# Optimization experiments

Hardware: AMD Instinct MI355X
Metric: run time of the kernel (lower is better)

Reference implementation:

```python
import jax, jax.numpy as jnp
import numpy as np
import math


def setup_inputs() -> dict:
    key = jax.random.key(0)
    ks = jax.random.split(key, 5)
    B, L, H = 16384, 336, 168
    T = L + H
    T_air = jax.random.normal(ks[0], (B, T), dtype=jnp.float32) * 8.0 + 10.0
    T_obs = T_air + jax.random.normal(ks[1], (B, T), dtype=jnp.float32) * 2.0
    wind = jax.random.uniform(ks[2], (B, T), dtype=jnp.float32) * 10.0
    par = jax.random.uniform(ks[3], (B, T), dtype=jnp.float32) * 500.0
    dt = jax.random.uniform(ks[4], (B, T), dtype=jnp.float32) * 3600.0 + 1800.0
    k_init = 1e-4
    k_raw = jnp.float32(k_init + math.log(-math.expm1(-k_init)))  # softplus inverse
    return {
        "T_obs": T_obs, "T_air": T_air, "wind": wind, "par": par, "dt": dt,
        "L_hist": L,
        "k_raw": k_raw,
        "log_q": jnp.float32(-8.0), "log_r": jnp.float32(-4.0),
        "log_p0": jnp.float32(-2.0), "log_q_scale": jnp.float32(0.0),
        "theta_par_lin": jnp.float32(1e-5), "theta_par_quad": jnp.float32(1e-8),
        "theta_wind_cool": jnp.float32(-1e-5), "theta_sensible": jnp.float32(-1e-6),
        "theta_forced_conv": jnp.float32(-1e-7),
    }


def reference(T_obs, T_air, wind, par, dt, L_hist, k_raw, log_q, log_r, log_p0,
              log_q_scale, theta_par_lin, theta_par_quad, theta_wind_cool,
              theta_sensible, theta_forced_conv):
    B, T_total = T_obs.shape
    L = int(L_hist)
    H = T_total - L

    k = jax.nn.softplus(k_raw)
    q = jnp.exp(log_q)
    q_scale = jnp.exp(log_q_scale)
    R = jnp.exp(log_r)
    P0 = jnp.exp(log_p0)

    def predict(T, P, Ta, w, p, dtt):
        dT = T - Ta
        cl = (theta_par_lin * p + theta_par_quad * p * p + theta_wind_cool * w
              + theta_sensible * dT + theta_forced_conv * w * dT)
        T_pred = jnp.clip(T - k * dT * dtt + cl * dtt, -50.0, 100.0)
        F = jnp.clip(1.0 - k * dtt + (theta_sensible + theta_forced_conv * w) * dtt, -2.0, 2.0)
        P_pred = jnp.clip(F * F * P + q_scale * q * dtt, 1e-10, 1e6)
        return T_pred, P_pred

    def filt_step(carry, xs):
        T, P = carry
        Ta, w, p, dtt, y = xs
        Tp, Pp = predict(T, P, Ta, w, p, dtt)
        S = Pp + R
        K = Pp / S
        T_upd = Tp + K * (y - Tp)
        P_upd = (1.0 - K) ** 2 * Pp + K * K * R
        return (T_upd, P_upd), None

    s0 = T_obs[:, 0]
    P0b = jnp.broadcast_to(P0, (B,)).astype(T_obs.dtype)

    # filtering over t = 1 .. L-1 (forcing from t-1, dt/obs at t)
    filt_xs = (T_air[:, :L - 1].T, wind[:, :L - 1].T, par[:, :L - 1].T,
               jnp.clip(dt[:, 1:L], 1.0, None).T, T_obs[:, 1:L].T)
    (s, P), _ = jax.lax.scan(filt_step, (s0, P0b), filt_xs)

    def fcst_step(carry, xs):
        T, P = carry
        Ta, w, p, dtt = xs
        Tp, Pp = predict(T, P, Ta, w, p, dtt)
        return (Tp, Pp), (Tp, Pp)

    # open-loop forecast over t = L .. L+H-1 (forcing from idx-1)
    fcst_xs = (T_air[:, L - 1:L + H - 1].T, wind[:, L - 1:L + H - 1].T,
               par[:, L - 1:L + H - 1].T, jnp.clip(dt[:, L:], 1.0, None).T)
    _, (T_preds, T_vars) = jax.lax.scan(fcst_step, (s, P), fcst_xs)

    return T_preds.T, T_vars.T  # each [B, H]
```

## Files before the change

kernel.cpp:

```cpp
#include <hip/hip_runtime.h>
#include <hip/hip_fp16.h>

namespace {
constexpr int kB = 16384;
constexpr int kL = 336;
constexpr int kH = 168;
constexpr int kT = 504;
constexpr int kW = 16;
constexpr int kNW = 32;
constexpr int kFW = 21;
constexpr int kNB = 4;
constexpr int kTP = 8;
constexpr int kS2 = 65;
constexpr int kTile2 = kTP * kS2;
constexpr int kOS = 17;
constexpr int kOT = 64 * kOS;
}

__device__ inline int fwaitc(int* f, int target, int cached) {
    if (cached >= target) { asm volatile("" ::: "memory"); return cached; }
    int v, guard = 0;
    while ((v = __hip_atomic_load(f, __ATOMIC_RELAXED, __HIP_MEMORY_SCOPE_WORKGROUP)) < target) {
        __builtin_amdgcn_s_sleep(1);
        if (++guard > (1 << 22)) { v = target; break; }
    }
    asm volatile("" ::: "memory");
    return v;
}
__device__ inline void fpost(int* f, int lane) {
    asm volatile("s_waitcnt lgkmcnt(0)" ::: "memory");
    if (lane == 0)
        __hip_atomic_fetch_add(f, 1, __ATOMIC_RELAXED, __HIP_MEMORY_SCOPE_WORKGROUP);
}

__global__ __launch_bounds__(256, 1)
void kf_fused(const float* __restrict__ g_obs,
              const float* __restrict__ g_air,
              const float* __restrict__ g_wind,
              const float* __restrict__ g_par,
              const float* __restrict__ g_dt,
              const float* __restrict__ s_k_raw,
              const float* __restrict__ s_log_q,
              const float* __restrict__ s_log_r,
              const float* __restrict__ s_log_p0,
              const float* __restrict__ s_log_qs,
              const float* __restrict__ s_th_pl,
              const float* __restrict__ s_th_pq,
              const float* __restrict__ s_th_wc,
              const float* __restrict__ s_th_s,
              const float* __restrict__ s_th_fc,
              float* __restrict__ out)
{
    __shared__ __half2 s_in[5][kNB][kTile2];
    __shared__ float   s_oT[2][kOT];
    __shared__ float   s_oV[2][kOT];
    __shared__ int     s_flag[8];

    const int tid = threadIdx.x, wid = tid >> 6, lane = tid & 63;
    const int b0 = blockIdx.x * 64;

    if (tid < 8) s_flag[tid] = 0;
    __syncthreads();

    int* pcAW = &s_flag[0];
    int* pcPD = &s_flag[1];
    int* pcY  = &s_flag[2];
    int* cc   = &s_flag[3];
    int* sc   = &s_flag[4];

    const int iq = lane & 3;
    const int ir = lane >> 2;

    auto issue = [&](const float* __restrict__ g, int w, float4* r) {
        int t = w * kW + iq * 4;
        if (t > kT - 4) t = kT - 4;
#pragma unroll
        for (int i = 0; i < 4; ++i)
            r[i] = *(const float4*)(g + (size_t)(b0 + 16 * i + ir) * kT + t);
    };
    auto stash = [&](const float4* r, __half2* dst) {
#pragma unroll
        for (int i = 0; i < 4; ++i) {
            const int row = 16 * i + ir;
            dst[(iq * 2    ) * kS2 + row] = __floats2half2_rn(r[i].x, r[i].y);
            dst[(iq * 2 + 1) * kS2 + row] = __floats2half2_rn(r[i].z, r[i].w);
        }
    };

    if (wid == 1 || wid == 2) {
        const float* g0 = (wid == 1) ? g_air  : g_par;
        const float* g1 = (wid == 1) ? g_wind : g_dt;
        __half2* t0b = (wid == 1) ? &s_in[0][0][0] : &s_in[2][0][0];
        __half2* t1b = (wid == 1) ? &s_in[1][0][0] : &s_in[3][0][0];
        int* pc = (wid == 1) ? pcAW : pcPD;

        float4 a0[4], c0[4], a1[4], c1[4];
        issue(g0, 0, a0); issue(g1, 0, c0);
        issue(g0, 1, a1); issue(g1, 1, c1);
        __builtin_amdgcn_sched_barrier(0);
        int vcc = 0;
        for (int w = 0; w < kNW; ++w) {
            if (w >= kNB) vcc = fwaitc(cc, w - (kNB - 1), vcc);
            const int bi = w & 3;
            if (w & 1) {
                stash(a1, t0b + bi * kTile2); stash(c1, t1b + bi * kTile2);
                fpost(pc, lane);
                if (w + 2 < kNW) { issue(g0, w + 2, a1); issue(g1, w + 2, c1); }
            } else {
                stash(a0, t0b + bi * kTile2); stash(c0, t1b + bi * kTile2);
                fpost(pc, lane);
                if (w + 2 < kNW) { issue(g0, w + 2, a0); issue(g1, w + 2, c0); }
            }
            __builtin_amdgcn_sched_barrier(0);
        }
    } else if (wid == 3) {
        __half2* yb = &s_in[4][0][0];
        float4 y0[4], y1[4];
        issue(g_obs, 0, y0); issue(g_obs, 1, y1);
        __builtin_amdgcn_sched_barrier(0);
        int vcc = 0;
        for (int w = 0; w < kFW; ++w) {
            if (w >= kNB) vcc = fwaitc(cc, w - (kNB - 1), vcc);
            const int bi = w & 3;
            if (w & 1) {
                stash(y1, yb + bi * kTile2);
                fpost(pcY, lane);
                if (w + 2 < kFW) issue(g_obs, w + 2, y1);
            } else {
                stash(y0, yb + bi * kTile2);
                fpost(pcY, lane);
                if (w + 2 < kFW) issue(g_obs, w + 2, y0);
            }
            __builtin_amdgcn_sched_barrier(0);
        }
        const int rq = lane & 3, rr = lane >> 2;
        float* outT = out;
        float* outV = out + (size_t)kB * kH;
        int vc2 = vcc;
        for (int w = kFW; w < kNW; ++w) {
            vc2 = fwaitc(cc, w + 1, vc2);
            const int ob = w & 1;
            const int h0 = (w - kFW) * kW;
            const int nq = (w == kNW - 1) ? 2 : 4;
#pragma unroll
            for (int i = 0; i < 4; ++i) {
                const int r = 16 * i + rr;
                if (rq < nq) {
                    const float4 tv = *(const float4*)&s_oT[ob][r * kOS + rq * 4];
                    const float4 vv = *(const float4*)&s_oV[ob][r * kOS + rq * 4];
                    *(float4*)&outT[(size_t)(b0 + r) * kH + h0 + rq * 4] = tv;
                    *(float4*)&outV[(size_t)(b0 + r) * kH + h0 + rq * 4] = vv;
                }
            }
            fpost(sc, lane);
        }
    } else {
        const float kpar = log1pf(expf(s_k_raw[0]));
        const float qq   = expf(s_log_q[0]) * expf(s_log_qs[0]);
        const float R    = expf(s_log_r[0]);
        float P          = expf(s_log_p0[0]);
        const float th_pl = s_th_pl[0], th_pq = s_th_pq[0], th_wc = s_th_wc[0];
        const float th_s  = s_th_s[0],  th_fc = s_th_fc[0];
        float Tst = 0.0f, aC = 0.0f, wC = 0.0f, pC = 0.0f;

        auto ks = [&](float ad, float wd, float pd, float D, float Y) {
            const float dtt = fmaxf(D, 1.0f);
            const float gk  = fmaf(th_fc, wd, th_s) - kpar;
            const float bs  = fmaf(pd, fmaf(th_pq, pd, th_pl), th_wc * wd);
            const float Fr  = fminf(fmaxf(fmaf(gk, dtt, 1.0f), -2.0f), 2.0f);
            const float Pp  = fminf(fmaxf(fmaf(Fr * Fr, P, qq * dtt), 1e-10f), 1e6f);
            const float Kg  = Pp * __builtin_amdgcn_rcpf(Pp + R);
            const float dT  = Tst - ad;
            const float Tp  = fminf(fmaxf(fmaf(fmaf(gk, dT, bs), dtt, Tst), -50.0f), 100.0f);
            Tst = fmaf(Kg, Y - Tp, Tp);
            const float omk = 1.0f - Kg;
            P = fmaf(omk * omk, Pp, Kg * Kg * R);
        };
        auto fs = [&](float ad, float wd, float pd, float D) {
            const float dtt = fmaxf(D, 1.0f);
            const float gk  = fmaf(th_fc, wd, th_s) - kpar;
            const float bs  = fmaf(pd, fmaf(th_pq, pd, th_pl), th_wc * wd);
            const float Fr  = fminf(fmaxf(fmaf(gk, dtt, 1.0f), -2.0f), 2.0f);
            P   = fminf(fmaxf(fmaf(Fr * Fr, P, qq * dtt), 1e-10f), 1e6f);
            const float dT  = Tst - ad;
            Tst = fminf(fmaxf(fmaf(fmaf(gk, dT, bs), dtt, Tst), -50.0f), 100.0f);
        };

        int vAW = 0, vPD = 0, vY = 0, vS = 0;
        for (int w = 0; w < kNW; ++w) {
            const int bi = w & 3;
            vAW = fwaitc(pcAW, w + 1, vAW);
            vPD = fwaitc(pcPD, w + 1, vPD);
            const bool filt = w < kFW;
            if (filt) vY = fwaitc(pcY, w + 1, vY);
            if (w >= kFW + 2) vS = fwaitc(sc, w - (kFW + 1), vS);

            const __half2* A2 = &s_in[0][bi][lane];
            const __half2* W2 = &s_in[1][bi][lane];
            const __half2* P2 = &s_in[2][bi][lane];
            const __half2* D2 = &s_in[3][bi][lane];
            const __half2* Y2 = &s_in[4][bi][lane];

            if (filt) {
                int tp0 = 0;
                if (w == 0) {
                    const float2 fa = __half22float2(A2[0]);
                    const float2 fw = __half22float2(W2[0]);
                    const float2 fp = __half22float2(P2[0]);
                    const float2 fd = __half22float2(D2[0]);
                    const float2 fy = __half22float2(Y2[0]);
                    Tst = fy.x;
                    ks(fa.x, fw.x, fp.x, fd.y, fy.y);
                    aC = fa.y; wC = fw.y; pC = fp.y;
                    tp0 = 1;
                }
#pragma unroll
                for (int tp = 0; tp < kTP; ++tp) {
                    if (tp < tp0) continue;
                    const float2 fa = __half22float2(A2[tp * kS2]);
                    const float2 fw = __half22float2(W2[tp * kS2]);
                    const float2 fp = __half22float2(P2[tp * kS2]);
                    const float2 fd = __half22float2(D2[tp * kS2]);
                    const float2 fy = __half22float2(Y2[tp * kS2]);
                    ks(aC,   wC,   pC,   fd.x, fy.x);
                    ks(fa.x, fw.x, fp.x, fd.y, fy.y);
                    aC = fa.y; wC = fw.y; pC = fp.y;
                }
            } else {
                const int ob = w & 1;
                float* oT = &s_oT[ob][lane * kOS];
                float* oV = &s_oV[ob][lane * kOS];
#pragma unroll
                for (int tp = 0; tp < kTP; ++tp) {
                    const float2 fa = __half22float2(A2[tp * kS2]);
                    const float2 fw = __half22float2(W2[tp * kS2]);
                    const float2 fp = __half22float2(P2[tp * kS2]);
                    const float2 fd = __half22float2(D2[tp * kS2]);
                    fs(aC,   wC,   pC,   fd.x); oT[2 * tp]     = Tst; oV[2 * tp]     = P;
                    fs(fa.x, fw.x, fp.x, fd.y); oT[2 * tp + 1] = Tst; oV[2 * tp + 1] = P;
                    aC = fa.y; wC = fw.y; pC = fp.y;
                }
            }
            fpost(cc, lane);
        }
    }
}

extern "C" void kernel_launch(void* const* d_in, const int* in_sizes, int n_in,
                              void* d_out, int out_size, void* d_ws, size_t ws_size,
                              hipStream_t stream) {
    const float* g_obs  = (const float*)d_in[0];
    const float* g_air  = (const float*)d_in[1];
    const float* g_wind = (const float*)d_in[2];
    const float* g_par  = (const float*)d_in[3];
    const float* g_dt   = (const float*)d_in[4];
    const float* k_raw  = (const float*)d_in[6];
    const float* log_q  = (const float*)d_in[7];
    const float* log_r  = (const float*)d_in[8];
    const float* log_p0 = (const float*)d_in[9];
    const float* log_qs = (const float*)d_in[10];
    const float* th_pl  = (const float*)d_in[11];
    const float* th_pq  = (const float*)d_in[12];
    const float* th_wc  = (const float*)d_in[13];
    const float* th_s   = (const float*)d_in[14];
    const float* th_fc  = (const float*)d_in[15];
    float* out = (float*)d_out;

    dim3 grid(kB / 64), block(256);
    hipLaunchKernelGGL(kf_fused, grid, block, 0, stream,
                       g_obs, g_air, g_wind, g_par, g_dt,
                       k_raw, log_q, log_r, log_p0, log_qs,
                       th_pl, th_pq, th_wc, th_s, th_fc, out);
}
```

Baseline: 220.3 us.

## Split Kalman recurrence into staged warps with precomputed affine coefficients

Restructures the warp-specialized pipeline into four stages. Two loader warps precompute per-step affine coefficients (A, B, F^2, q*dt) from the forcing data. A variance warp runs the scalar P/Kalman-gain recurrence, and a state warp runs a T recurrence reduced to one fma and a clamp per step. The staging buffers move from fp16 to fp32, which removes precision loss but doubles shared-memory traffic. Outputs are written directly from the recurrence warps instead of going through a separate writer warp. The goal is to shorten the serial dependency chain on the critical path by splitting the independent P and T recurrences across warps, at the cost of more inter-warp flag synchronization.

```diff
diff --git a/kernel.cpp b/kernel.cpp
--- a/kernel.cpp
+++ b/kernel.cpp
@@ -1,5 +1,4 @@
 #include <hip/hip_runtime.h>
-#include <hip/hip_fp16.h>
 
 namespace {
 constexpr int kB = 16384;
@@ -10,11 +9,10 @@
 constexpr int kNW = 32;
 constexpr int kFW = 21;
 constexpr int kNB = 4;
-constexpr int kTP = 8;
-constexpr int kS2 = 65;
-constexpr int kTile2 = kTP * kS2;
-constexpr int kOS = 17;
-constexpr int kOT = 64 * kOS;
+constexpr int kTSa = 69;
+constexpr int kTS2 = 65;
+constexpr int kTileA = kW * kTSa;
+constexpr int kTile2 = kW * kTS2;
 }
 
 __device__ inline int fwaitc(int* f, int target, int cached) {
@@ -51,10 +49,12 @@
               const float* __restrict__ s_th_fc,
               float* __restrict__ out)
 {
-    __shared__ __half2 s_in[5][kNB][kTile2];
-    __shared__ float   s_oT[2][kOT];
-    __shared__ float   s_oV[2][kOT];
-    __shared__ int     s_flag[8];
+    __shared__ float  s_A [kNB][kTileA];
+    __shared__ float  s_K [kNB][kTileA];
+    __shared__ float2 s_DC[kNB][kTile2];
+    __shared__ float2 s_VQ[kNB][kTile2];
+    __shared__ float2 s_BY[kNB][kTile2];
+    __shared__ int    s_flag[8];
 
     const int tid = threadIdx.x, wid = tid >> 6, lane = tid & 63;
     const int b0 = blockIdx.x * 64;
@@ -62,11 +62,10 @@
     if (tid < 8) s_flag[tid] = 0;
     __syncthreads();
 
-    int* pcAW = &s_flag[0];
-    int* pcPD = &s_flag[1];
-    int* pcY  = &s_flag[2];
-    int* cc   = &s_flag[3];
-    int* sc   = &s_flag[4];
+    int* f0 = &s_flag[0];
+    int* f1 = &s_flag[1];
+    int* f2 = &s_flag[2];
+    int* f3 = &s_flag[3];
 
     const int iq = lane & 3;
     const int ir = lane >> 2;
@@ -78,170 +77,196 @@
         for (int i = 0; i < 4; ++i)
             r[i] = *(const float4*)(g + (size_t)(b0 + 16 * i + ir) * kT + t);
     };
-    auto stash = [&](const float4* r, __half2* dst) {
-#pragma unroll
-        for (int i = 0; i < 4; ++i) {
-            const int row = 16 * i + ir;
-            dst[(iq * 2    ) * kS2 + row] = __floats2half2_rn(r[i].x, r[i].y);
-            dst[(iq * 2 + 1) * kS2 + row] = __floats2half2_rn(r[i].z, r[i].w);
-        }
-    };
-
-    if (wid == 1 || wid == 2) {
-        const float* g0 = (wid == 1) ? g_air  : g_par;
-        const float* g1 = (wid == 1) ? g_wind : g_dt;
-        __half2* t0b = (wid == 1) ? &s_in[0][0][0] : &s_in[2][0][0];
-        __half2* t1b = (wid == 1) ? &s_in[1][0][0] : &s_in[3][0][0];
-        int* pc = (wid == 1) ? pcAW : pcPD;
-
-        float4 a0[4], c0[4], a1[4], c1[4];
-        issue(g0, 0, a0); issue(g1, 0, c0);
-        issue(g0, 1, a1); issue(g1, 1, c1);
+
+    if (wid == 0) {
+        const float kpar  = log1pf(expf(s_k_raw[0]));
+        const float R     = expf(s_log_r[0]);
+        const float qq    = expf(s_log_q[0]) * expf(s_log_qs[0]);
+        const float th_wc = s_th_wc[0], th_fc = s_th_fc[0];
+        const float th_sk = s_th_s[0] - kpar;
+
+        float4 wA[4], dA[4], wB[4], dB[4];
+        issue(g_wind, 0, wA); issue(g_dt, 0, dA);
+        issue(g_wind, 1, wB); issue(g_dt, 1, dB);
         __builtin_amdgcn_sched_barrier(0);
-        int vcc = 0;
-        for (int w = 0; w < kNW; ++w) {
-            if (w >= kNB) vcc = fwaitc(cc, w - (kNB - 1), vcc);
-            const int bi = w & 3;
-            if (w & 1) {
-                stash(a1, t0b + bi * kTile2); stash(c1, t1b + bi * kTile2);
-                fpost(pc, lane);
-                if (w + 2 < kNW) { issue(g0, w + 2, a1); issue(g1, w + 2, c1); }
+        float cw[4] = {0.f, 0.f, 0.f, 0.f};
+        int v2 = 0, v3 = 0;
+        for (int w = 0; w < kNW; ++w) {
+            if (w >= kNB) {
+                v2 = fwaitc(f2, w - (kNB - 1), v2);
+                v3 = fwaitc(f3, w - (kNB - 1), v3);
+            }
+            const int bi = w & 3;
+            const float sel = (w < kFW) ? R : 1.0f;
+            float4* wq = (w & 1) ? wB : wA;
+            float4* dq = (w & 1) ? dB : dA;
+#pragma unroll
+            for (int i = 0; i < 4; ++i) {
+                const float4 wv = wq[i], dv = dq[i];
+                const float fl = __shfl(wv.w, lane - 1);
+                const float fc = __shfl(cw[i], lane | 3);
+                float wp[4], dt4[4] = {dv.x, dv.y, dv.z, dv.w};
+                wp[0] = (iq == 0) ? fc : fl;
+                wp[1] = wv.x; wp[2] = wv.y; wp[3] = wv.z;
+                cw[i] = wv.w;
+                const int rb = 16 * i + ir;
+#pragma unroll
+                for (int j = 0; j < 4; ++j) {
+                    const int tl = iq * 4 + j;
+                    const float dtt = fmaxf(dt4[j], 1.0f);
+                    const float gk  = fmaf(th_fc, wp[j], th_sk);
+                    const float A   = fmaf(gk, dtt, 1.0f);
+                    const float Fr  = fminf(fmaxf(A, -2.0f), 2.0f);
+                    const float V2  = Fr * Fr * sel;
+                    const float qd  = qq * dtt;
+                    const float c3  = (th_wc * wp[j]) * dtt;
+                    s_A [bi][tl * kTSa + rb] = A;
+                    s_DC[bi][tl * kTS2 + rb] = make_float2(dtt, c3);
+                    s_VQ[bi][tl * kTS2 + rb] = make_float2(V2, qd);
+                }
+            }
+            fpost(f0, lane);
+            if (w + 2 < kNW) {
+                if (w & 1) { issue(g_wind, w + 2, wB); issue(g_dt, w + 2, dB); }
+                else       { issue(g_wind, w + 2, wA); issue(g_dt, w + 2, dA); }
+            }
+            __builtin_amdgcn_sched_barrier(0);
+        }
+    } else if (wid == 1) {
+        const float th_pl = s_th_pl[0], th_pq = s_th_pq[0];
+        float4 aA[4], pA[4], yA[4], aB[4], pB[4], yB[4];
+        issue(g_air, 0, aA); issue(g_par, 0, pA); issue(g_obs, 0, yA);
+        issue(g_air, 1, aB); issue(g_par, 1, pB); issue(g_obs, 1, yB);
+        __builtin_amdgcn_sched_barrier(0);
+        float ca[4] = {0.f, 0.f, 0.f, 0.f}, cp[4] = {0.f, 0.f, 0.f, 0.f};
+        int v0 = 0, v3 = 0;
+        for (int w = 0; w < kNW; ++w) {
+            v0 = fwaitc(f0, w + 1, v0);
+            if (w >= kNB) v3 = fwaitc(f3, w - (kNB - 1), v3);
+            const int bi = w & 3;
+            float4* aq = (w & 1) ? aB : aA;
+            float4* pq = (w & 1) ? pB : pA;
+            float4* yq = (w & 1) ? yB : yA;
+#pragma unroll
+            for (int i = 0; i < 4; ++i) {
+                const float4 av = aq[i], pv = pq[i], yv = yq[i];
+                const float fla = __shfl(av.w, lane - 1), fca = __shfl(ca[i], lane | 3);
+                const float flp = __shfl(pv.w, lane - 1), fcp = __shfl(cp[i], lane | 3);
+                float ap[4] = {(iq == 0) ? fca : fla, av.x, av.y, av.z};
+                float pp[4] = {(iq == 0) ? fcp : flp, pv.x, pv.y, pv.z};
+                float y4[4] = {yv.x, yv.y, yv.z, yv.w};
+                ca[i] = av.w; cp[i] = pv.w;
+                const int rb = 16 * i + ir;
+#pragma unroll
+                for (int j = 0; j < 4; ++j) {
+                    const int tl = iq * 4 + j;
+                    const float2 dc = s_DC[bi][tl * kTS2 + rb];
+                    const float A   = s_A [bi][tl * kTSa + rb];
+                    const float c1  = A - 1.0f;
+                    const float pbs = pp[j] * fmaf(th_pq, pp[j], th_pl);
+                    const float B   = fmaf(pbs, dc.x, dc.y) - c1 * ap[j];
+                    s_BY[bi][tl * kTS2 + rb] = make_float2(B, y4[j]);
+                }
+            }
+            fpost(f1, lane);
+            if (w + 2 < kNW) {
+                if (w & 1) { issue(g_air, w + 2, aB); issue(g_par, w + 2, pB);
+                             if (w + 2 < kFW) issue(g_obs, w + 2, yB); }
+                else       { issue(g_air, w + 2, aA); issue(g_par, w + 2, pA);
+                             if (w + 2 < kFW) issue(g_obs, w + 2, yA); }
+            }
+            __builtin_amdgcn_sched_barrier(0);
+        }
+    } else if (wid == 2) {
+        const float R  = expf(s_log_r[0]);
+        const float P0 = expf(s_log_p0[0]);
+        float kg = P0 / R;
+        float P  = 0.0f;
+        float* outV = out + (size_t)kB * kH;
+        const int row = b0 + lane;
+        int v0 = 0, v3 = 0;
+        for (int w = 0; w < kNW; ++w) {
+            v0 = fwaitc(f0, w + 1, v0);
+            if (w >= kNB) v3 = fwaitc(f3, w - (kNB - 1), v3);
+            const int bi = w & 3;
+            float2 vq[kW];
+#pragma unroll
+            for (int t = 0; t < kW; ++t) vq[t] = s_VQ[bi][t * kTS2 + lane];
+            if (w < kFW) {
+#pragma unroll
+                for (int t = 0; t < kW; ++t) {
+                    if (w == 0 && t == 0) continue;
+                    float Pp = fmaf(vq[t].x, kg, vq[t].y);
+                    Pp = fminf(fmaxf(Pp, 1e-10f), 1e6f);
+                    kg = Pp * __builtin_amdgcn_rcpf(Pp + R);
+                    s_K[bi][t * kTSa + lane] = kg;
+                }
             } else {
-                stash(a0, t0b + bi * kTile2); stash(c0, t1b + bi * kTile2);
-                fpost(pc, lane);
-                if (w + 2 < kNW) { issue(g0, w + 2, a0); issue(g1, w + 2, c0); }
-            }
-            __builtin_amdgcn_sched_barrier(0);
-        }
-    } else if (wid == 3) {
-        __half2* yb = &s_in[4][0][0];
-        float4 y0[4], y1[4];
-        issue(g_obs, 0, y0); issue(g_obs, 1, y1);
-        __builtin_amdgcn_sched_barrier(0);
-        int vcc = 0;
-        for (int w = 0; w < kFW; ++w) {
-            if (w >= kNB) vcc = fwaitc(cc, w - (kNB - 1), vcc);
-            const int bi = w & 3;
-            if (w & 1) {
-                stash(y1, yb + bi * kTile2);
-                fpost(pcY, lane);
-                if (w + 2 < kFW) issue(g_obs, w + 2, y1);
+                if (w == kFW) P = R * kg;
+                float o[kW];
+#pragma unroll
+                for (int t = 0; t < kW; ++t) {
+                    P = fminf(fmaxf(fmaf(vq[t].x, P, vq[t].y), 1e-10f), 1e6f);
+                    o[t] = P;
+                }
+                const int hb = (w - kFW) * kW;
+                const int nq = (w == kNW - 1) ? 2 : 4;
+#pragma unroll
+                for (int qn = 0; qn < 4; ++qn)
+                    if (qn < nq)
+                        *(float4*)&outV[(size_t)row * kH + hb + 4 * qn] =
+                            make_float4(o[4*qn], o[4*qn+1], o[4*qn+2], o[4*qn+3]);
+            }
+            fpost(f2, lane);
+        }
+    } else {
+        float Tst = 0.0f;
+        float* outT = out;
+        const int row = b0 + lane;
+        int v1 = 0, v2 = 0;
+        for (int w = 0; w < kNW; ++w) {
+            v1 = fwaitc(f1, w + 1, v1);
+            const int bi = w & 3;
+            if (w < kFW) {
+                v2 = fwaitc(f2, w + 1, v2);
+                float2 by[kW]; float Av[kW], kgv[kW];
+#pragma unroll
+                for (int t = 0; t < kW; ++t) {
+                    by[t]  = s_BY[bi][t * kTS2 + lane];
+                    Av[t]  = s_A [bi][t * kTSa + lane];
+                    kgv[t] = s_K [bi][t * kTSa + lane];
+                }
+                if (w == 0) Tst = by[0].y;
+#pragma unroll
+                for (int t = 0; t < kW; ++t) {
+                    if (w == 0 && t == 0) continue;
+                    float Tp = fmaf(Av[t], Tst, by[t].x);
+                    Tp = fminf(fmaxf(Tp, -50.0f), 100.0f);
+                    Tst = fmaf(1.0f - kgv[t], Tp, kgv[t] * by[t].y);
+                }
             } else {
-                stash(y0, yb + bi * kTile2);
-                fpost(pcY, lane);
-                if (w + 2 < kFW) issue(g_obs, w + 2, y0);
-            }
-            __builtin_amdgcn_sched_barrier(0);
-        }
-        const int rq = lane & 3, rr = lane >> 2;
-        float* outT = out;
-        float* outV = out + (size_t)kB * kH;
-        int vc2 = vcc;
-        for (int w = kFW; w < kNW; ++w) {
-            vc2 = fwaitc(cc, w + 1, vc2);
-            const int ob = w & 1;
-            const int h0 = (w - kFW) * kW;
-            const int nq = (w == kNW - 1) ? 2 : 4;
-#pragma unroll
-            for (int i = 0; i < 4; ++i) {
-                const int r = 16 * i + rr;
-                if (rq < nq) {
-                    const float4 tv = *(const float4*)&s_oT[ob][r * kOS + rq * 4];
-                    const float4 vv = *(const float4*)&s_oV[ob][r * kOS + rq * 4];
-                    *(float4*)&outT[(size_t)(b0 + r) * kH + h0 + rq * 4] = tv;
-                    *(float4*)&outV[(size_t)(b0 + r) * kH + h0 + rq * 4] = vv;
-                }
-            }
-            fpost(sc, lane);
-        }
-    } else {
-        const float kpar = log1pf(expf(s_k_raw[0]));
-        const float qq   = expf(s_log_q[0]) * expf(s_log_qs[0]);
-        const float R    = expf(s_log_r[0]);
-        float P          = expf(s_log_p0[0]);
-        const float th_pl = s_th_pl[0], th_pq = s_th_pq[0], th_wc = s_th_wc[0];
-        const float th_s  = s_th_s[0],  th_fc = s_th_fc[0];
-        float Tst = 0.0f, aC = 0.0f, wC = 0.0f, pC = 0.0f;
-
-        auto ks = [&](float ad, float wd, float pd, float D, float Y) {
-            const float dtt = fmaxf(D, 1.0f);
-            const float gk  = fmaf(th_fc, wd, th_s) - kpar;
-            const float bs  = fmaf(pd, fmaf(th_pq, pd, th_pl), th_wc * wd);
-            const float Fr  = fminf(fmaxf(fmaf(gk, dtt, 1.0f), -2.0f), 2.0f);
-            const float Pp  = fminf(fmaxf(fmaf(Fr * Fr, P, qq * dtt), 1e-10f), 1e6f);
-            const float Kg  = Pp * __builtin_amdgcn_rcpf(Pp + R);
-            const float dT  = Tst - ad;
-            const float Tp  = fminf(fmaxf(fmaf(fmaf(gk, dT, bs), dtt, Tst), -50.0f), 100.0f);
-            Tst = fmaf(Kg, Y - Tp, Tp);
-            const float omk = 1.0f - Kg;
-            P = fmaf(omk * omk, Pp, Kg * Kg * R);
-        };
-        auto fs = [&](float ad, float wd, float pd, float D) {
-            const float dtt = fmaxf(D, 1.0f);
-            const float gk  = fmaf(th_fc, wd, th_s) - kpar;
-            const float bs  = fmaf(pd, fmaf(th_pq, pd, th_pl), th_wc * wd);
-            const float Fr  = fminf(fmaxf(fmaf(gk, dtt, 1.0f), -2.0f), 2.0f);
-            P   = fminf(fmaxf(fmaf(Fr * Fr, P, qq * dtt), 1e-10f), 1e6f);
-            const float dT  = Tst - ad;
-            Tst = fminf(fmaxf(fmaf(fmaf(gk, dT, bs), dtt, Tst), -50.0f), 100.0f);
-        };
-
-        int vAW = 0, vPD = 0, vY = 0, vS = 0;
-        for (int w = 0; w < kNW; ++w) {
-            const int bi = w & 3;
-            vAW = fwaitc(pcAW, w + 1, vAW);
-            vPD = fwaitc(pcPD, w + 1, vPD);
-            const bool filt = w < kFW;
-            if (filt) vY = fwaitc(pcY, w + 1, vY);
-            if (w >= kFW + 2) vS = fwaitc(sc, w - (kFW + 1), vS);
-
-            const __half2* A2 = &s_in[0][bi][lane];
-            const __half2* W2 = &s_in[1][bi][lane];
-            const __half2* P2 = &s_in[2][bi][lane];
-            const __half2* D2 = &s_in[3][bi][lane];
-            const __half2* Y2 = &s_in[4][bi][lane];
-
-            if (filt) {
-                int tp0 = 0;
-                if (w == 0) {
-                    const float2 fa = __half22float2(A2[0]);
-                    const float2 fw = __half22float2(W2[0]);
-                    const float2 fp = __half22float2(P2[0]);
-                    const float2 fd = __half22float2(D2[0]);
-                    const float2 fy = __half22float2(Y2[0]);
-                    Tst = fy.x;
-                    ks(fa.x, fw.x, fp.x, fd.y, fy.y);
-                    aC = fa.y; wC = fw.y; pC = fp.y;
-                    tp0 = 1;
-                }
-#pragma unroll
-                for (int tp = 0; tp < kTP; ++tp) {
-                    if (tp < tp0) continue;
-                    const float2 fa = __half22float2(A2[tp * kS2]);
-                    const float2 fw = __half22float2(W2[tp * kS2]);
-                    const float2 fp = __half22float2(P2[tp * kS2]);
-                    const float2 fd = __half22float2(D2[tp * kS2]);
-                    const float2 fy = __half22float2(Y2[tp * kS2]);
-                    ks(aC,   wC,   pC,   fd.x, fy.x);
-                    ks(fa.x, fw.x, fp.x, fd.y, fy.y);
-                    aC = fa.y; wC = fw.y; pC = fp.y;
-                }
-            } else {
-                const int ob = w & 1;
-                float* oT = &s_oT[ob][lane * kOS];
-                float* oV = &s_oV[ob][lane * kOS];
-#pragma unroll
-                for (int tp = 0; tp < kTP; ++tp) {
-                    const float2 fa = __half22float2(A2[tp * kS2]);
-                    const float2 fw = __half22float2(W2[tp * kS2]);
-                    const float2 fp = __half22float2(P2[tp * kS2]);
-                    const float2 fd = __half22float2(D2[tp * kS2]);
-                    fs(aC,   wC,   pC,   fd.x); oT[2 * tp]     = Tst; oV[2 * tp]     = P;
-                    fs(fa.x, fw.x, fp.x, fd.y); oT[2 * tp + 1] = Tst; oV[2 * tp + 1] = P;
-                    aC = fa.y; wC = fw.y; pC = fp.y;
-                }
-            }
-            fpost(cc, lane);
+                float2 by[kW]; float Av[kW];
+#pragma unroll
+                for (int t = 0; t < kW; ++t) {
+                    by[t] = s_BY[bi][t * kTS2 + lane];
+                    Av[t] = s_A [bi][t * kTSa + lane];
+                }
+                float o[kW];
+#pragma unroll
+                for (int t = 0; t < kW; ++t) {
+                    float Tp = fmaf(Av[t], Tst, by[t].x);
+                    Tst = fminf(fmaxf(Tp, -50.0f), 100.0f);
+                    o[t] = Tst;
+                }
+                const int hb = (w - kFW) * kW;
+                const int nq = (w == kNW - 1) ? 2 : 4;
+#pragma unroll
+                for (int qn = 0; qn < 4; ++qn)
+                    if (qn < nq)
+                        *(float4*)&outT[(size_t)row * kH + hb + 4 * qn] =
+                            make_float4(o[4*qn], o[4*qn+1], o[4*qn+2], o[4*qn+3]);
+            }
+            fpost(f3, lane);
         }
     }
 }
```

Measured after the change: 246.4 us. +11.8%, slower.
